# Kernel tuning notes

Measured on AMD Instinct MI355X. Metric: run time of the kernel, lower is better.

Reference implementation:

```python
import jax, jax.numpy as jnp
import numpy as np
from jax import lax

D_MODEL, D_INNER, D_STATE, D_CONV, DT_RANK = 128, 256, 16, 4, 8
BATCH, SEQ = 8, 4096


def setup_inputs() -> dict:
    key = jax.random.key(0)
    ks = jax.random.split(key, 13)
    g = lambda k, shape, fan: (jax.random.normal(k, shape, jnp.float32) / np.sqrt(fan)).astype(jnp.float32)
    inp = {
        "s": jax.random.normal(ks[0], (BATCH, SEQ, D_MODEL), jnp.float32),
        "in_proj_w": g(ks[1], (2 * D_INNER, D_MODEL), D_MODEL),
        "conv_w": g(ks[2], (D_INNER, 1, D_CONV), D_CONV),
        "conv_b": jnp.zeros((D_INNER,), jnp.float32),
        "x_proj_w": g(ks[3], (DT_RANK + 2 * D_STATE, D_INNER), D_INNER),
        "dt_proj_w": g(ks[4], (D_INNER, DT_RANK), DT_RANK),
        "dt_proj_b": jax.random.uniform(ks[5], (D_INNER,), jnp.float32, -4.0, -2.0),  # softplus(b) small, like mamba dt init
        "A_log": jnp.log(jnp.broadcast_to(jnp.arange(1, D_STATE + 1, dtype=jnp.float32), (D_INNER, D_STATE))),
        "D_skip": jnp.ones((D_INNER,), jnp.float32),
        "out_proj_w": g(ks[6], (D_MODEL, D_INNER), D_INNER),
        "ln_gamma": jnp.ones((D_MODEL,), jnp.float32),
        "ln_beta": jnp.zeros((D_MODEL,), jnp.float32),
        "fc_w": g(ks[7], (D_MODEL, D_MODEL), D_MODEL),
    }
    return inp


def _mamba(s, in_proj_w, conv_w, conv_b, x_proj_w, dt_proj_w, dt_proj_b, A_log, D_skip, out_proj_w):
    B, L, _ = s.shape
    xz = jnp.einsum("bld,ed->ble", s, in_proj_w)           # [B,L,2*D_INNER]
    x, z = jnp.split(xz, 2, axis=-1)                        # each [B,L,D_INNER]
    # causal depthwise conv1d
    xc = jnp.transpose(x, (0, 2, 1))                        # [B,D_INNER,L]
    xc = jnp.pad(xc, ((0, 0), (0, 0), (D_CONV - 1, 0)))
    xc = lax.conv_general_dilated(xc, conv_w, (1,), "VALID",
                                  dimension_numbers=("NCH", "OIH", "NCH"),
                                  feature_group_count=D_INNER)
    x = jax.nn.silu(jnp.transpose(xc + conv_b[None, :, None], (0, 2, 1)))  # [B,L,D_INNER]
    # input-dependent dt, B, C
    x_dbl = jnp.einsum("bld,ed->ble", x, x_proj_w)
    dt = x_dbl[..., :DT_RANK]
    Bc = x_dbl[..., DT_RANK:DT_RANK + D_STATE]              # [B,L,D_STATE]
    Cc = x_dbl[..., DT_RANK + D_STATE:]                     # [B,L,D_STATE]
    dt = jax.nn.softplus(jnp.einsum("blr,dr->bld", dt, dt_proj_w) + dt_proj_b)  # [B,L,D_INNER]
    A = -jnp.exp(A_log)                                     # [D_INNER,D_STATE]

    def step(h, inp):
        dt_t, b_t, c_t, u_t = inp                           # [B,Di],[B,Ds],[B,Ds],[B,Di]
        dA = jnp.exp(dt_t[:, :, None] * A)                  # [B,Di,Ds]
        dBu = (dt_t * u_t)[:, :, None] * b_t[:, None, :]
        h = dA * h + dBu
        y = jnp.einsum("bds,bs->bd", h, c_t)
        return h, y

    h0 = jnp.zeros((B, D_INNER, D_STATE), x.dtype)
    xs = (jnp.swapaxes(dt, 0, 1), jnp.swapaxes(Bc, 0, 1), jnp.swapaxes(Cc, 0, 1), jnp.swapaxes(x, 0, 1))
    _, ys = lax.scan(step, h0, xs)                          # ys: [L,B,D_INNER]
    y = jnp.swapaxes(ys, 0, 1) + x * D_skip
    y = y * jax.nn.silu(z)
    return jnp.einsum("bld,od->blo", y, out_proj_w)         # [B,L,D_MODEL]


def reference(s, in_proj_w, conv_w, conv_b, x_proj_w, dt_proj_w, dt_proj_b, A_log, D_skip, out_proj_w, ln_gamma, ln_beta, fc_w):
    h = _mamba(s, in_proj_w, conv_w, conv_b, x_proj_w, dt_proj_w, dt_proj_b, A_log, D_skip, out_proj_w)
    mu = jnp.mean(h, axis=-1, keepdims=True)
    var = jnp.mean(jnp.square(h - mu), axis=-1, keepdims=True)
    hn = (h - mu) * lax.rsqrt(var + 1e-5) * ln_gamma + ln_beta
    return jax.nn.relu(jnp.einsum("bld,od->blo", hn, fc_w))
```

## Files before the change

### kernel.cpp

```cpp
#include <hip/hip_runtime.h>
#include <math.h>

#define B_ 8
#define L_ 4096
#define DM 128
#define DI 256
#define DSN 16
#define RK 8
#define M_ (B_*L_)
#define NC 128
#define CH 32
#define CH2 64

typedef __attribute__((ext_vector_type(8))) short bfrag;
typedef __attribute__((ext_vector_type(4))) float ffrag;
typedef __attribute__((ext_vector_type(2))) float f32x2;

__device__ __forceinline__ float silu_f(float x) {
  return x * __builtin_amdgcn_rcpf(1.f + __expf(-x));
}
__device__ __forceinline__ float softplus_f(float x) {
  return (x > 20.f) ? x : __logf(1.f + __expf(x));
}

__device__ __forceinline__ unsigned short f2bf(float f) {
  unsigned int u = __builtin_bit_cast(unsigned int, f);
  unsigned int r = (u + 0x7FFFu + ((u >> 16) & 1u)) >> 16;
  return (unsigned short)r;
}
__device__ __forceinline__ unsigned int f2bf2(float lo, float hi) {
  return (unsigned int)f2bf(lo) | ((unsigned int)f2bf(hi) << 16);
}
__device__ __forceinline__ float bf2f(unsigned int us) {
  return __builtin_bit_cast(float, us << 16);
}

__global__ __launch_bounds__(256)
void prep_weights(const float* __restrict__ w_in, const float* __restrict__ xw,
                  const float* __restrict__ ow, const float* __restrict__ fcw,
                  unsigned short* __restrict__ w_in_b, unsigned short* __restrict__ xw_b,
                  unsigned short* __restrict__ ow_b, unsigned short* __restrict__ fcw_b) {
  const int i = blockIdx.x * 256 + threadIdx.x;
  const float* src; unsigned short* dst; int j;
  if (i < 16384)      { src = w_in; dst = w_in_b; j = i; }
  else if (i < 18944) { src = xw;   dst = xw_b;   j = i - 16384; }
  else if (i < 27136) { src = ow;   dst = ow_b;   j = i - 18944; }
  else if (i < 31232) { src = fcw;  dst = fcw_b;  j = i - 27136; }
  else return;
  float4 v = *(const float4*)&src[j << 2];
  uint2 p = {f2bf2(v.x, v.y), f2bf2(v.z, v.w)};
  *(uint2*)&dst[j << 2] = p;
}

__global__ __launch_bounds__(256, 4)
void xproj_dtproj(const float* __restrict__ s, const unsigned short* __restrict__ w_in_b,
                  const unsigned short* __restrict__ xw_b,
                  const float* __restrict__ dtw, const float* __restrict__ dtpb,
                  const float* __restrict__ cw, const float* __restrict__ cb,
                  const float* __restrict__ alog,
                  float* __restrict__ Bb, float* __restrict__ Cb,
                  unsigned int* __restrict__ udt,
                  unsigned short* __restrict__ zsb,
                  unsigned short* __restrict__ cP, unsigned short* __restrict__ cHe) {
  __shared__ __align__(16) char pool[38960];
  unsigned short* As = (unsigned short*)pool;
  unsigned short* ua = (unsigned short*)pool;
  unsigned short* hx = (unsigned short*)(pool + 16896);
  float* dtr_s = (float*)(pool + 35376);
  float* Bs_l  = (float*)(pool + 36912);
  const int t = threadIdx.x;
  const int p0 = blockIdx.x << 5;
  const int w = t >> 6, l = t & 63, q = l >> 4, col = l & 15;

  for (int i = t; i < 48 * 32; i += 256) {
    int row = i >> 5, c4 = i & 31;
    int pos = (row < 32) ? (p0 + row) : (p0 - 16 + (row - 32));
    if (pos < 0) pos = 0;
    float4 av = *(const float4*)&s[pos * 128 + (c4 << 2)];
    uint2 ap = {f2bf2(av.x, av.y), f2bf2(av.z, av.w)};
    *(uint2*)&As[row * 136 + (c4 << 2)] = ap;
  }
  __syncthreads();
  for (int jt = 0; jt < 8; ++jt) {
    const int wrow0 = jt << 6;
    const int T = (jt < 4) ? 12 : 8;
    for (int tile = w; tile < T; tile += 4) {
      const int mt = tile >> 2, nt = tile & 3;
      ffrag acc = {0.f, 0.f, 0.f, 0.f};
#pragma unroll
      for (int s8 = 0; s8 < 4; ++s8) {
        int k0 = s8 * 32 + q * 8;
        bfrag af = *(const bfrag*)&As[((mt << 4) + col) * 136 + k0];
        bfrag wf = *(const bfrag*)&w_in_b[(wrow0 + (nt << 4) + col) * 128 + k0];
        acc = __builtin_amdgcn_mfma_f32_16x16x32_bf16(wf, af, acc, 0, 0, 0);
      }
      const int chb = (nt << 4) + (q << 2);
      if (jt < 4) {
        uint2 pk = {f2bf2(acc[0], acc[1]), f2bf2(acc[2], acc[3])};
        const int ch = (jt << 6) + chb;
        if (mt < 2) {
          *(uint2*)&hx[(3 + (mt << 4) + col) * 264 + ch] = pk;
        } else if (col >= 13) {
          *(uint2*)&hx[(col - 13) * 264 + ch] = pk;
        }
      } else {
        uint2 pk = {f2bf2(silu_f(acc[0]), silu_f(acc[1])),
                    f2bf2(silu_f(acc[2]), silu_f(acc[3]))};
        const int m = p0 + (mt << 4) + col;
        *(uint2*)&zsb[m * 256 + ((jt - 4) << 6) + chb] = pk;
      }
    }
  }
  __syncthreads();
  {
    const int k = t;
    const int lb = p0 & (L_ - 1);
    const float w0 = cw[k*4], w1 = cw[k*4+1], w2 = cw[k*4+2], w3 = cw[k*4+3];
    const float bias = cb[k];
    float x0 = (lb >= 3) ? bf2f((unsigned int)hx[0 * 264 + k]) : 0.f;
    float x1 = (lb >= 2) ? bf2f((unsigned int)hx[1 * 264 + k]) : 0.f;
    float x2 = (lb >= 1) ? bf2f((unsigned int)hx[2 * 264 + k]) : 0.f;
#pragma unroll 8
    for (int it = 0; it < 32; ++it) {
      float x3 = bf2f((unsigned int)hx[(3 + it) * 264 + k]);
      float u = silu_f(fmaf(w0, x0, fmaf(w1, x1, fmaf(w2, x2, fmaf(w3, x3, bias)))));
      ua[it * 264 + k] = f2bf(u);
      x0 = x1; x1 = x2; x2 = x3;
    }
  }
  __syncthreads();
  for (int tile = w; tile < 6; tile += 4) {
    const int mt = tile & 1, nt = tile >> 1;
    ffrag acc = {0.f, 0.f, 0.f, 0.f};
#pragma unroll
    for (int s8 = 0; s8 < 8; ++s8) {
      int k0 = s8 * 32 + q * 8;
      bfrag af = *(const bfrag*)&ua[((mt << 4) + col) * 264 + k0];
      const int nrow = (nt << 4) + col;
      bfrag wf = {0, 0, 0, 0, 0, 0, 0, 0};
      if (nrow < 40) wf = *(const bfrag*)&xw_b[nrow * 256 + k0];
      acc = __builtin_amdgcn_mfma_f32_16x16x32_bf16(wf, af, acc, 0, 0, 0);
    }
    const int ml = (mt << 4) + col;
    const int m = p0 + ml;
    const int n0 = (nt << 4) + (q << 2);
    float4 v = {acc[0], acc[1], acc[2], acc[3]};
    if (n0 < 8) {
      *(float4*)&dtr_s[ml * 12 + n0] = v;
    } else if (n0 < 24) {
      *(float4*)&Bb[m * 16 + (n0 - 8)] = v;
      *(float4*)&Bs_l[ml * 16 + (n0 - 8)] = v;
    } else if (n0 < 40) {
      *(float4*)&Cb[m * 16 + (n0 - 24)] = v;
    }
  }
  __syncthreads();
  {
    const int d = t;
    const int bb = p0 >> 12;
    const int cc = (p0 & (L_ - 1)) >> 5;
    const int bc = bb * NC + cc;
    float w8[8];
    *(float4*)&w8[0] = *(const float4*)&dtw[d * 8];
    *(float4*)&w8[4] = *(const float4*)&dtw[d * 8 + 4];
    const float bias = dtpb[d];
    float a[16];
    bool okl = true;
#pragma unroll
    for (int j = 0; j < 16; ++j) {
      a[j] = -__expf(alog[d * 16 + j]);
      float tgt = (float)(j + 1);
      okl = okl && (fabsf(a[j] + tgt) <= 1e-3f * tgt);
    }
    const bool fast = (bool)__all((int)okl);
    f32x2 h2[8] = {{0.f,0.f},{0.f,0.f},{0.f,0.f},{0.f,0.f},
                   {0.f,0.f},{0.f,0.f},{0.f,0.f},{0.f,0.f}};
    float sdt = 0.f;
#pragma unroll 2
    for (int pp = 0; pp < 32; ++pp) {
      float r0[8];
      *(float4*)&r0[0] = *(const float4*)&dtr_s[pp * 12];
      *(float4*)&r0[4] = *(const float4*)&dtr_s[pp * 12 + 4];
      float a2 = bias;
#pragma unroll
      for (int r2 = 0; r2 < 8; ++r2) a2 = fmaf(r0[r2], w8[r2], a2);
      float sp = softplus_f(a2);
      unsigned int uq = (unsigned int)ua[pp * 264 + d];
      unsigned short spb = f2bf(sp);
      udt[(p0 + pp) * 256 + d] = uq | ((unsigned int)spb << 16);
      float dtv = bf2f((unsigned int)spb);
      float uv  = bf2f(uq);
      float du = dtv * uv;
      sdt += dtv;
      const float* brow = &Bs_l[pp * 16];
      float4 b0 = *(const float4*)&brow[0];
      float4 b1 = *(const float4*)&brow[4];
      float4 b2 = *(const float4*)&brow[8];
      float4 b3 = *(const float4*)&brow[12];
      f32x2 B2[8] = {{b0.x,b0.y},{b0.z,b0.w},{b1.x,b1.y},{b1.z,b1.w},
                     {b2.x,b2.y},{b2.z,b2.w},{b3.x,b3.y},{b3.z,b3.w}};
      f32x2 du2 = {du, du};
      if (fast) {
        float e1 = __expf(-dtv);
        float e2 = e1 * e1;
        f32x2 dA = {e1, e2};
        f32x2 e22 = {e2, e2};
#pragma unroll
        for (int jj = 0; jj < 8; ++jj) {
          h2[jj] = dA * h2[jj] + du2 * B2[jj];
          dA = dA * e22;
        }
      } else {
#pragma unroll
        for (int j = 0; j < 16; ++j) {
          float dA = __expf(dtv * a[j]);
          h2[j >> 1][j & 1] = fmaf(dA, h2[j >> 1][j & 1], du * B2[j >> 1][j & 1]);
        }
      }
    }
#pragma unroll
    for (int j = 0; j < 16; ++j) {
      int o = (bc * 16 + j) * 256 + d;
      cP[o]  = f2bf(__expf(a[j] * sdt));
      cHe[o] = f2bf(h2[j >> 1][j & 1]);
    }
  }
}

__global__ __launch_bounds__(512)
void scan_combine(unsigned short* __restrict__ cP, const unsigned short* __restrict__ cHe) {
  __shared__ float segP[64 * 9], segH[64 * 9], segS[64 * 9];
  const int t = threadIdx.x;
  const int sdl = t & 63, seg = t >> 6;
  const int blk = blockIdx.x;
  const int b = blk >> 6, grp = blk & 63;
  const int sd = (grp << 6) + sdl;
  const int base = b * NC * 4096 + sd;
  float Pacc = 1.f, Hacc = 0.f;
#pragma unroll
  for (int i = 0; i < 16; ++i) {
    int idx = base + (seg * 16 + i) * 4096;
    float p = bf2f((unsigned int)cP[idx]);
    float he = bf2f((unsigned int)cHe[idx]);
    Hacc = fmaf(p, Hacc, he);
    Pacc *= p;
  }
  segP[sdl * 9 + seg] = Pacc;
  segH[sdl * 9 + seg] = Hacc;
  __syncthreads();
  if (t < 64) {
    float hs = 0.f;
#pragma unroll
    for (int s2 = 0; s2 < 8; ++s2) {
      segS[t * 9 + s2] = hs;
      hs = fmaf(segP[t * 9 + s2], hs, segH[t * 9 + s2]);
    }
  }
  __syncthreads();
  float hs = segS[sdl * 9 + seg];
#pragma unroll
  for (int i = 0; i < 16; ++i) {
    int idx = base + (seg * 16 + i) * 4096;
    float p = bf2f((unsigned int)cP[idx]);
    float he = bf2f((unsigned int)cHe[idx]);
    cP[idx] = f2bf(hs);
    hs = fmaf(p, hs, he);
  }
}

__global__ __launch_bounds__(512, 4)
void scan3_out_ln_fc(const unsigned int* __restrict__ udt,
                     const float* __restrict__ Bb, const float* __restrict__ Cb,
                     const float* __restrict__ alog, const unsigned short* __restrict__ hst,
                     const float* __restrict__ dsk,
                     const unsigned short* __restrict__ zsb,
                     const unsigned short* __restrict__ ow_b,
                     const float* __restrict__ gamma, const float* __restrict__ beta,
                     const unsigned short* __restrict__ fcw_b, float* __restrict__ out) {
  __shared__ float Bs[CH2 * 16];
  __shared__ float Cs[CH2 * 16];
  __shared__ unsigned short smA[64 * 264];
  __shared__ unsigned short smB[128 * 136];
  __shared__ float pS1[128], pS2[128];
  const int bc = blockIdx.x;
  const int b = bc >> 6, cc = bc & 63;
  const int t = threadIdx.x;
  const int l = t & 63, w = t >> 6;
  const int chh = t >> 8;
  const int d = t & 255;
  const int base = b * L_ + (cc << 1) * CH;
  const int cbase = base + chh * CH;
  const int hc = b * NC + (cc << 1) + chh;
  if (t < CH2 * 4)           ((float4*)Bs)[t]            = *(const float4*)&Bb[base * 16 + (t << 2)];
  else if (t < CH2 * 8)      ((float4*)Cs)[t - CH2 * 4]  = *(const float4*)&Cb[base * 16 + ((t - CH2 * 4) << 2)];
  float a[16];
  bool okl = true;
#pragma unroll
  for (int j = 0; j < 16; ++j) {
    a[j] = -__expf(alog[d * 16 + j]);
    float tgt = (float)(j + 1);
    okl = okl && (fabsf(a[j] + tgt) <= 1e-3f * tgt);
  }
  const bool fast = (bool)__all((int)okl);
  const float dskv = dsk[d];
  f32x2 h2[8];
#pragma unroll
  for (int jj = 0; jj < 8; ++jj) {
    h2[jj][0] = bf2f((unsigned int)hst[(hc * 16 + (jj << 1)) * 256 + d]);
    h2[jj][1] = bf2f((unsigned int)hst[(hc * 16 + (jj << 1) + 1) * 256 + d]);
  }
  unsigned int wv0 = udt[cbase * 256 + d];
  unsigned int wv1 = udt[(cbase + 1) * 256 + d];
  unsigned short zv0 = zsb[cbase * 256 + d];
  unsigned short zv1 = zsb[(cbase + 1) * 256 + d];
  __syncthreads();
#pragma unroll 2
  for (int ll = 0; ll < CH; ++ll) {
    const int l2 = (ll + 2 < CH) ? ll + 2 : CH - 1;
    unsigned int wv2 = udt[(cbase + l2) * 256 + d];
    unsigned short zv2 = zsb[(cbase + l2) * 256 + d];
    const float* brow = &Bs[(chh * CH + ll) * 16];
    const float* crow = &Cs[(chh * CH + ll) * 16];
    float4 b0 = *(const float4*)&brow[0];
    float4 b1 = *(const float4*)&brow[4];
    float4 b2 = *(const float4*)&brow[8];
    float4 b3 = *(const float4*)&brow[12];
    float4 c0 = *(const float4*)&crow[0];
    float4 c1 = *(const float4*)&crow[4];
    float4 c2 = *(const float4*)&crow[8];
    float4 c3 = *(const float4*)&crow[12];
    float uv  = bf2f(wv0 & 0xFFFFu);
    float dtv = bf2f(wv0 >> 16);
    f32x2 B2[8] = {{b0.x,b0.y},{b0.z,b0.w},{b1.x,b1.y},{b1.z,b1.w},
                   {b2.x,b2.y},{b2.z,b2.w},{b3.x,b3.y},{b3.z,b3.w}};
    f32x2 C2[8] = {{c0.x,c0.y},{c0.z,c0.w},{c1.x,c1.y},{c1.z,c1.w},
                   {c2.x,c2.y},{c2.z,c2.w},{c3.x,c3.y},{c3.z,c3.w}};
    float du = dtv * uv;
    f32x2 du2 = {du, du};
    f32x2 y2 = {0.f, 0.f};
    if (fast) {
      float e1 = __expf(-dtv);
      float e2 = e1 * e1;
      f32x2 dA = {e1, e2};
      f32x2 e22 = {e2, e2};
#pragma unroll
      for (int jj = 0; jj < 8; ++jj) {
        h2[jj] = dA * h2[jj] + du2 * B2[jj];
        y2 = y2 + h2[jj] * C2[jj];
        dA = dA * e22;
      }
    } else {
#pragma unroll
      for (int j = 0; j < 16; ++j) {
        float dA = __expf(dtv * a[j]);
        float hh = fmaf(dA, h2[j >> 1][j & 1], du * B2[j >> 1][j & 1]);
        h2[j >> 1][j & 1] = hh;
        y2[j & 1] = fmaf(hh, C2[j >> 1][j & 1], y2[j & 1]);
      }
    }
    float y = y2.x + y2.y;
    float zs = bf2f((unsigned int)zv0);
    smA[(chh * CH + ll) * 264 + d] = f2bf(fmaf(uv, dskv, y) * zs);
    wv0 = wv1; wv1 = wv2; zv0 = zv1; zv1 = zv2;
  }
  const int q = l >> 4, col = l & 15;
  const int rw = w & 3, np = w >> 2;
  ffrag acc[2][2];
  for (int nt2 = 0; nt2 < 2; ++nt2) {
    __syncthreads();
    for (int i = t; i < 64 * 32; i += 512) {
      int row = i >> 5, c8 = (i & 31) << 3;
      *(uint4*)&smB[row * 264 + c8] = *(const uint4*)&ow_b[((nt2 << 6) + row) * 256 + c8];
    }
    __syncthreads();
#pragma unroll
    for (int nt = 0; nt < 2; ++nt) acc[nt2][nt] = (ffrag){0.f, 0.f, 0.f, 0.f};
#pragma unroll
    for (int s8 = 0; s8 < 8; ++s8) {
      int k0 = s8 * 32 + q * 8;
      bfrag af = *(const bfrag*)&smA[((rw << 4) + col) * 264 + k0];
#pragma unroll
      for (int nt = 0; nt < 2; ++nt) {
        bfrag bf_ = *(const bfrag*)&smB[((((np << 1) + nt) << 4) + col) * 264 + k0];
        acc[nt2][nt] = __builtin_amdgcn_mfma_f32_16x16x32_bf16(af, bf_, acc[nt2][nt], 0, 0, 0);
      }
    }
  }
  float s1v[4], s2v[4];
#pragma unroll
  for (int i = 0; i < 4; ++i) {
    float s1 = 0.f, s2 = 0.f;
#pragma unroll
    for (int nt2 = 0; nt2 < 2; ++nt2)
#pragma unroll
      for (int nt = 0; nt < 2; ++nt) {
        float v = acc[nt2][nt][i];
        s1 += v; s2 = fmaf(v, v, s2);
      }
    s1 += __shfl_xor(s1, 1); s2 += __shfl_xor(s2, 1);
    s1 += __shfl_xor(s1, 2); s2 += __shfl_xor(s2, 2);
    s1 += __shfl_xor(s1, 4); s2 += __shfl_xor(s2, 4);
    s1 += __shfl_xor(s1, 8); s2 += __shfl_xor(s2, 8);
    s1v[i] = s1; s2v[i] = s2;
  }
  if (col == 0) {
#pragma unroll
    for (int i = 0; i < 4; ++i) {
      int r = (rw << 4) + (q << 2) + i;
      pS1[(np << 6) + r] = s1v[i];
      pS2[(np << 6) + r] = s2v[i];
    }
  }
  __syncthreads();
  float mu[4], rs[4];
#pragma unroll
  for (int i = 0; i < 4; ++i) {
    int r = (rw << 4) + (q << 2) + i;
    float s1 = pS1[r] + pS1[64 + r];
    float s2 = pS2[r] + pS2[64 + r];
    mu[i] = s1 * (1.f / DM);
    float var = s2 * (1.f / DM) - mu[i] * mu[i];
    rs[i] = rsqrtf(var + 1e-5f);
  }
#pragma unroll
  for (int nt2 = 0; nt2 < 2; ++nt2)
#pragma unroll
    for (int nt = 0; nt < 2; ++nt) {
      int n = (nt2 << 6) + ((((np << 1) + nt)) << 4) + col;
      float g = gamma[n], be = beta[n];
#pragma unroll
      for (int i = 0; i < 4; ++i) {
        int r = (rw << 4) + (q << 2) + i;
        smA[r * 136 + n] = f2bf(fmaf((acc[nt2][nt][i] - mu[i]) * rs[i], g, be));
      }
    }
  for (int i = t; i < 128 * 16; i += 512) {
    int row = i >> 4, c8 = (i & 15) << 3;
    *(uint4*)&smB[row * 136 + c8] = *(const uint4*)&fcw_b[row * 128 + c8];
  }
  __syncthreads();
  ffrag a2[4] = {{0.f,0.f,0.f,0.f},{0.f,0.f,0.f,0.f},{0.f,0.f,0.f,0.f},{0.f,0.f,0.f,0.f}};
#pragma unroll
  for (int s8 = 0; s8 < 4; ++s8) {
    int k0 = s8 * 32 + q * 8;
    bfrag af = *(const bfrag*)&smA[((rw << 4) + col) * 136 + k0];
#pragma unroll
    for (int nt = 0; nt < 4; ++nt) {
      bfrag bf_ = *(const bfrag*)&smB[((((np << 2) + nt) << 4) + col) * 136 + k0];
      a2[nt] = __builtin_amdgcn_mfma_f32_16x16x32_bf16(af, bf_, a2[nt], 0, 0, 0);
    }
  }
#pragma unroll
  for (int nt = 0; nt < 4; ++nt)
#pragma unroll
    for (int i = 0; i < 4; ++i) {
      int ml = (rw << 4) + (q << 2) + i;
      out[(base + ml) * 128 + (((np << 2) + nt) << 4) + col] = fmaxf(a2[nt][i], 0.f);
    }
}

extern "C" void kernel_launch(void* const* d_in, const int* in_sizes, int n_in,
                              void* d_out, int out_size, void* d_ws, size_t ws_size,
                              hipStream_t stream) {
  (void)in_sizes; (void)n_in; (void)out_size; (void)ws_size;
  const float* s    = (const float*)d_in[0];
  const float* w_in = (const float*)d_in[1];
  const float* cw   = (const float*)d_in[2];
  const float* cb   = (const float*)d_in[3];
  const float* xw   = (const float*)d_in[4];
  const float* dtw  = (const float*)d_in[5];
  const float* dtpb = (const float*)d_in[6];
  const float* alog = (const float*)d_in[7];
  const float* dsk  = (const float*)d_in[8];
  const float* ow   = (const float*)d_in[9];
  const float* gam  = (const float*)d_in[10];
  const float* bet  = (const float*)d_in[11];
  const float* fcw  = (const float*)d_in[12];
  float* out = (float*)d_out;
  float* ws  = (float*)d_ws;

  unsigned short* zsb  = (unsigned short*)(ws + 4194304);
  unsigned int*   udt  = (unsigned int*)(ws + 8388608);
  float*          Bb   = ws + 16777216;
  float*          Cb   = ws + 17301504;
  unsigned short* cP   = (unsigned short*)(ws + 17825792);
  unsigned short* cHe  = (unsigned short*)(ws + 19922944);
  unsigned short* w_in_b = (unsigned short*)(ws + 22020096);
  unsigned short* xw_b   = (unsigned short*)(ws + 22052864);
  unsigned short* ow_b   = (unsigned short*)(ws + 22057984);
  unsigned short* fcw_b  = (unsigned short*)(ws + 22074368);

  prep_weights<<<122, 256, 0, stream>>>(w_in, xw, ow, fcw, w_in_b, xw_b, ow_b, fcw_b);
  xproj_dtproj<<<M_ / CH, 256, 0, stream>>>(s, w_in_b, xw_b, dtw, dtpb, cw, cb, alog,
                                            Bb, Cb, udt, zsb, cP, cHe);
  scan_combine<<<512, 512, 0, stream>>>(cP, cHe);
  scan3_out_ln_fc<<<B_ * NC / 2, 512, 0, stream>>>(udt, Bb, Cb, alog, cP, dsk, zsb,
                                                   ow_b, gam, bet, fcw_b, out);
}
```

Measured before the change: 167.0 us.

## Fold dt_proj into x_proj weights and compute dt via MFMA

Result: slower. 190.5 us (+14.1%).

```diff
diff --git a/kernel.cpp b/kernel.cpp
--- a/kernel.cpp
+++ b/kernel.cpp
@@ -38,36 +38,55 @@
 __global__ __launch_bounds__(256)
 void prep_weights(const float* __restrict__ w_in, const float* __restrict__ xw,
                   const float* __restrict__ ow, const float* __restrict__ fcw,
+                  const float* __restrict__ dtw,
                   unsigned short* __restrict__ w_in_b, unsigned short* __restrict__ xw_b,
-                  unsigned short* __restrict__ ow_b, unsigned short* __restrict__ fcw_b) {
+                  unsigned short* __restrict__ ow_b, unsigned short* __restrict__ fcw_b,
+                  unsigned short* __restrict__ Mb) {
   const int i = blockIdx.x * 256 + threadIdx.x;
-  const float* src; unsigned short* dst; int j;
-  if (i < 16384)      { src = w_in; dst = w_in_b; j = i; }
-  else if (i < 18944) { src = xw;   dst = xw_b;   j = i - 16384; }
-  else if (i < 27136) { src = ow;   dst = ow_b;   j = i - 18944; }
-  else if (i < 31232) { src = fcw;  dst = fcw_b;  j = i - 27136; }
-  else return;
-  float4 v = *(const float4*)&src[j << 2];
-  uint2 p = {f2bf2(v.x, v.y), f2bf2(v.z, v.w)};
-  *(uint2*)&dst[j << 2] = p;
+  if (i < 31232) {
+    const float* src; unsigned short* dst; int j;
+    if (i < 16384)      { src = w_in; dst = w_in_b; j = i; }
+    else if (i < 18944) { src = xw;   dst = xw_b;   j = i - 16384; }
+    else if (i < 27136) { src = ow;   dst = ow_b;   j = i - 18944; }
+    else                { src = fcw;  dst = fcw_b;  j = i - 27136; }
+    float4 v = *(const float4*)&src[j << 2];
+    uint2 p = {f2bf2(v.x, v.y), f2bf2(v.z, v.w)};
+    *(uint2*)&dst[j << 2] = p;
+  } else if (i < 47616) {
+    const int j = i - 31232;
+    const int dch = j >> 6;
+    const int k4 = (j & 63) << 2;
+    float m0 = 0.f, m1 = 0.f, m2 = 0.f, m3 = 0.f;
+#pragma unroll
+    for (int r = 0; r < 8; ++r) {
+      float wv = dtw[dch * 8 + r];
+      const float* xr = &xw[r * 256 + k4];
+      m0 = fmaf(wv, xr[0], m0);
+      m1 = fmaf(wv, xr[1], m1);
+      m2 = fmaf(wv, xr[2], m2);
+      m3 = fmaf(wv, xr[3], m3);
+    }
+    uint2 p = {f2bf2(m0, m1), f2bf2(m2, m3)};
+    *(uint2*)&Mb[dch * 256 + k4] = p;
+  }
 }
 
 __global__ __launch_bounds__(256, 4)
 void xproj_dtproj(const float* __restrict__ s, const unsigned short* __restrict__ w_in_b,
                   const unsigned short* __restrict__ xw_b,
-                  const float* __restrict__ dtw, const float* __restrict__ dtpb,
+                  const unsigned short* __restrict__ Mb,
+                  const float* __restrict__ dtpb,
                   const float* __restrict__ cw, const float* __restrict__ cb,
                   const float* __restrict__ alog,
                   float* __restrict__ Bb, float* __restrict__ Cb,
                   unsigned int* __restrict__ udt,
                   unsigned short* __restrict__ zsb,
                   unsigned short* __restrict__ cP, unsigned short* __restrict__ cHe) {
-  __shared__ __align__(16) char pool[38960];
+  __shared__ __align__(16) char pool[37424];
   unsigned short* As = (unsigned short*)pool;
   unsigned short* ua = (unsigned short*)pool;
   unsigned short* hx = (unsigned short*)(pool + 16896);
-  float* dtr_s = (float*)(pool + 35376);
-  float* Bs_l  = (float*)(pool + 36912);
+  float* Bs_l  = (float*)(pool + 35376);
   const int t = threadIdx.x;
   const int p0 = blockIdx.x << 5;
   const int w = t >> 6, l = t & 63, q = l >> 4, col = l & 15;
@@ -129,29 +148,44 @@
     }
   }
   __syncthreads();
-  for (int tile = w; tile < 6; tile += 4) {
-    const int mt = tile & 1, nt = tile >> 1;
+  for (int tile = w; tile < 36; tile += 4) {
+    const int mt = tile & 1, ntv = tile >> 1;
+    const unsigned short* wsrc = (ntv < 2)
+        ? &xw_b[(8 + (ntv << 4) + col) * 256]
+        : &Mb[((((ntv - 2) << 4) + col)) * 256];
     ffrag acc = {0.f, 0.f, 0.f, 0.f};
 #pragma unroll
     for (int s8 = 0; s8 < 8; ++s8) {
       int k0 = s8 * 32 + q * 8;
       bfrag af = *(const bfrag*)&ua[((mt << 4) + col) * 264 + k0];
-      const int nrow = (nt << 4) + col;
-      bfrag wf = {0, 0, 0, 0, 0, 0, 0, 0};
-      if (nrow < 40) wf = *(const bfrag*)&xw_b[nrow * 256 + k0];
+      bfrag wf = *(const bfrag*)&wsrc[k0];
       acc = __builtin_amdgcn_mfma_f32_16x16x32_bf16(wf, af, acc, 0, 0, 0);
     }
-    const int ml = (mt << 4) + col;
-    const int m = p0 + ml;
-    const int n0 = (nt << 4) + (q << 2);
-    float4 v = {acc[0], acc[1], acc[2], acc[3]};
-    if (n0 < 8) {
-      *(float4*)&dtr_s[ml * 12 + n0] = v;
-    } else if (n0 < 24) {
-      *(float4*)&Bb[m * 16 + (n0 - 8)] = v;
-      *(float4*)&Bs_l[ml * 16 + (n0 - 8)] = v;
-    } else if (n0 < 40) {
-      *(float4*)&Cb[m * 16 + (n0 - 24)] = v;
+    const int pos = (mt << 4) + col;
+    const int m = p0 + pos;
+    if (ntv < 2) {
+      const int n0 = (ntv << 4) + (q << 2);
+      float4 v = {acc[0], acc[1], acc[2], acc[3]};
+      if (n0 < 16) {
+        *(float4*)&Bb[m * 16 + n0] = v;
+        *(float4*)&Bs_l[pos * 16 + n0] = v;
+      } else {
+        *(float4*)&Cb[m * 16 + (n0 - 16)] = v;
+      }
+    } else {
+      const int ch = ((ntv - 2) << 4) + (q << 2);
+      float4 bia = *(const float4*)&dtpb[ch];
+      float d0 = softplus_f(acc[0] + bia.x);
+      float d1 = softplus_f(acc[1] + bia.y);
+      float d2 = softplus_f(acc[2] + bia.z);
+      float d3 = softplus_f(acc[3] + bia.w);
+      unsigned long long uq4 = *(const unsigned long long*)&ua[pos * 264 + ch];
+      uint4 pk;
+      pk.x = (unsigned int)(unsigned short)(uq4)       | ((unsigned int)f2bf(d0) << 16);
+      pk.y = (unsigned int)(unsigned short)(uq4 >> 16) | ((unsigned int)f2bf(d1) << 16);
+      pk.z = (unsigned int)(unsigned short)(uq4 >> 32) | ((unsigned int)f2bf(d2) << 16);
+      pk.w = (unsigned int)(unsigned short)(uq4 >> 48) | ((unsigned int)f2bf(d3) << 16);
+      *(uint4*)&udt[m * 256 + ch] = pk;
     }
   }
   __syncthreads();
@@ -160,10 +194,6 @@
     const int bb = p0 >> 12;
     const int cc = (p0 & (L_ - 1)) >> 5;
     const int bc = bb * NC + cc;
-    float w8[8];
-    *(float4*)&w8[0] = *(const float4*)&dtw[d * 8];
-    *(float4*)&w8[4] = *(const float4*)&dtw[d * 8 + 4];
-    const float bias = dtpb[d];
     float a[16];
     bool okl = true;
 #pragma unroll
@@ -176,20 +206,14 @@
     f32x2 h2[8] = {{0.f,0.f},{0.f,0.f},{0.f,0.f},{0.f,0.f},
                    {0.f,0.f},{0.f,0.f},{0.f,0.f},{0.f,0.f}};
     float sdt = 0.f;
+    unsigned int wv0 = udt[(p0 + 0) * 256 + d];
+    unsigned int wv1 = udt[(p0 + 1) * 256 + d];
 #pragma unroll 2
     for (int pp = 0; pp < 32; ++pp) {
-      float r0[8];
-      *(float4*)&r0[0] = *(const float4*)&dtr_s[pp * 12];
-      *(float4*)&r0[4] = *(const float4*)&dtr_s[pp * 12 + 4];
-      float a2 = bias;
-#pragma unroll
-      for (int r2 = 0; r2 < 8; ++r2) a2 = fmaf(r0[r2], w8[r2], a2);
-      float sp = softplus_f(a2);
-      unsigned int uq = (unsigned int)ua[pp * 264 + d];
-      unsigned short spb = f2bf(sp);
-      udt[(p0 + pp) * 256 + d] = uq | ((unsigned int)spb << 16);
-      float dtv = bf2f((unsigned int)spb);
-      float uv  = bf2f(uq);
+      const int p2 = (pp + 2 < 32) ? pp + 2 : 31;
+      unsigned int wv2 = udt[(p0 + p2) * 256 + d];
+      float uv  = bf2f(wv0 & 0xFFFFu);
+      float dtv = bf2f(wv0 >> 16);
       float du = dtv * uv;
       sdt += dtv;
       const float* brow = &Bs_l[pp * 16];
@@ -217,6 +241,7 @@
           h2[j >> 1][j & 1] = fmaf(dA, h2[j >> 1][j & 1], du * B2[j >> 1][j & 1]);
         }
       }
+      wv0 = wv1; wv1 = wv2;
     }
 #pragma unroll
     for (int j = 0; j < 16; ++j) {
@@ -489,9 +514,11 @@
   unsigned short* xw_b   = (unsigned short*)(ws + 22052864);
   unsigned short* ow_b   = (unsigned short*)(ws + 22057984);
   unsigned short* fcw_b  = (unsigned short*)(ws + 22074368);
-
-  prep_weights<<<122, 256, 0, stream>>>(w_in, xw, ow, fcw, w_in_b, xw_b, ow_b, fcw_b);
-  xproj_dtproj<<<M_ / CH, 256, 0, stream>>>(s, w_in_b, xw_b, dtw, dtpb, cw, cb, alog,
+  unsigned short* Mb     = (unsigned short*)(ws + 22082560);
+
+  prep_weights<<<186, 256, 0, stream>>>(w_in, xw, ow, fcw, dtw,
+                                        w_in_b, xw_b, ow_b, fcw_b, Mb);
+  xproj_dtproj<<<M_ / CH, 256, 0, stream>>>(s, w_in_b, xw_b, Mb, dtpb, cw, cb, alog,
                                             Bb, Cb, udt, zsb, cP, cHe);
   scan_combine<<<512, 512, 0, stream>>>(cP, cHe);
   scan3_out_ln_fc<<<B_ * NC / 2, 512, 0, stream>>>(udt, Bb, Cb, alog, cP, dsk, zsb,
```
